# Optimization experiments

Measured on AMD Instinct MI355X. Metric: run time of the kernel, lower is better.

## Reference

```python
import jax, jax.numpy as jnp
import numpy as np

NHEAD = 8
LN_EPS = 1e-5   # torch nn.LayerNorm default
ATT_EPS = 1e-6  # LinearAttention eps


def layernorm(x, g, b):
    mu = jnp.mean(x, axis=-1, keepdims=True)
    var = jnp.mean((x - mu) ** 2, axis=-1, keepdims=True)
    return (x - mu) / jnp.sqrt(var + LN_EPS) * g + b


def setup_inputs() -> dict:
    key = jax.random.key(0)
    ks = jax.random.split(key, 9)
    B, C, H, W = 8, 256, 64, 64
    d = C
    w = lambda k, shp: (jax.random.normal(k, shp, dtype=jnp.float32) * 0.02)
    return {
        "x": jax.random.normal(ks[0], (B, C, H, W), dtype=jnp.float32),
        "source": jax.random.normal(ks[1], (B, C, H, W), dtype=jnp.float32),
        # weights stored [in, out] (already transposed vs torch's [out, in])
        "Wq": w(ks[2], (d, d)),
        "Wk": w(ks[3], (d, d)),
        "Wv": w(ks[4], (d, d)),
        "Wm": w(ks[5], (d, d)),
        "W1": w(ks[6], (2 * d, 2 * d)),
        "W2": w(ks[7], (2 * d, d)),
        "g1": jnp.ones((d,), jnp.float32),
        "b1": jnp.zeros((d,), jnp.float32),
        "g2": jnp.ones((d,), jnp.float32),
        "b2": jnp.zeros((d,), jnp.float32),
    }


def reference(x, source, Wq, Wk, Wv, Wm, W1, W2, g1, b1, g2, b2):
    B, C, H, W = x.shape
    L = H * W
    dim = C // NHEAD
    xs = x.reshape(B, C, L).transpose(0, 2, 1)        # [B, L, C]
    ss = source.reshape(B, C, L).transpose(0, 2, 1)   # [B, L, C]

    q = (xs @ Wq).reshape(B, L, NHEAD, dim)
    k = (ss @ Wk).reshape(B, L, NHEAD, dim)
    v = (ss @ Wv).reshape(B, L, NHEAD, dim)

    # linear attention with elu+1 feature map
    Q = jax.nn.elu(q) + 1.0
    K = jax.nn.elu(k) + 1.0
    vals = v / L
    KV = jnp.einsum('nshd,nshv->nhdv', K, vals)                    # [B, h, d, d]
    Z = 1.0 / (jnp.einsum('nlhd,nhd->nlh', Q, K.sum(axis=1)) + ATT_EPS)
    msg = jnp.einsum('nlhd,nhdv,nlh->nlhv', Q, KV, Z) * L          # [B, L, h, d]

    msg = msg.reshape(B, L, C) @ Wm
    msg = layernorm(msg, g1, b1)
    msg = jax.nn.relu(jnp.concatenate([xs, msg], axis=-1) @ W1) @ W2
    msg = layernorm(msg, g2, b2)

    out = xs + msg
    return out.transpose(0, 2, 1).reshape(B, C, H, W)
```

## Files before the change

### kernel.cpp

```cpp
#include <hip/hip_runtime.h>

typedef unsigned short u16;
typedef __bf16 bf16x8 __attribute__((ext_vector_type(8)));
typedef float f32x4 __attribute__((ext_vector_type(4)));

__device__ __forceinline__ u16 f2bf(float f) {
  unsigned int u = __float_as_uint(f);
  u += 0x7fffu + ((u >> 16) & 1u);
  return (u16)(u >> 16);
}
__device__ __forceinline__ float bf2f(u16 v) {
  return __uint_as_float(((unsigned)v) << 16);
}

#define GLDS16(gp, lp)                                                   \
  __builtin_amdgcn_global_load_lds(                                      \
      (const __attribute__((address_space(1))) unsigned int*)(gp),       \
      (__attribute__((address_space(3))) unsigned int*)(lp), 16, 0, 0)

#define OFF_WQ     0u
#define OFF_WK     131072u
#define OFF_WV     262144u
#define OFF_WM     393216u
#define OFF_W1     524288u
// ... 23 lines not shown
  __syncthreads();
#pragma unroll
  for (int i = 0; i < 4; ++i)
    dst[((size_t)b * 4096 + lt + ty + i * 8) * dstride + ct + tx] = f2bf(s[tx][ty + i * 8]);
}

__global__ __launch_bounds__(256) void wprep_all_kernel(
    const float* __restrict__ Wq, const float* __restrict__ Wk,
    const float* __restrict__ Wv, const float* __restrict__ Wm,
    const float* __restrict__ W1, const float* __restrict__ W2,
    u16* __restrict__ dq, u16* __restrict__ dk, u16* __restrict__ dv,
    u16* __restrict__ dm, u16* __restrict__ d1, u16* __restrict__ d2) {
  __shared__ float s[32][33];
  int bid = blockIdx.x;
  const float* src; u16* dst; int Kd, Nd, t;
  if (bid < 64)       { src = Wq; dst = dq; Kd = 256; Nd = 256; t = bid; }
  else if (bid < 128) { src = Wk; dst = dk; Kd = 256; Nd = 256; t = bid - 64; }
  else if (bid < 192) { src = Wv; dst = dv; Kd = 256; Nd = 256; t = bid - 128; }
  else if (bid < 256) { src = Wm; dst = dm; Kd = 256; Nd = 256; t = bid - 192; }
  else if (bid < 512) { src = W1; dst = d1; Kd = 512; Nd = 512; t = bid - 256; }
  else                { src = W2; dst = d2; Kd = 512; Nd = 256; t = bid - 512; }
  int ntn = Nd >> 5;
  int kt = (t / ntn) * 32, nt = (t % ntn) * 32;
  int tx = threadIdx.x & 31, ty = threadIdx.x >> 5;
#pragma unroll
  for (int i = 0; i < 4; ++i)
    s[ty + i * 8][tx] = src[(size_t)(kt + ty + i * 8) * Nd + nt + tx];
  __syncthreads();
#pragma unroll
  for (int i = 0; i < 4; ++i)
    dst[(size_t)(nt + ty + i * 8) * Kd + kt + tx] = f2bf(s[tx][ty + i * 8]);
}

template <int EPI, int XS>
__global__ __launch_bounds__(256) void gemm_kernel(
    const u16* __restrict__ A, int lda, const u16* __restrict__ Wt, int K,
    u16* __restrict__ outp, int ldo) {
  __shared__ alignas(16) u16 sA[128 * 64];
  __shared__ alignas(16) u16 sB[128 * 64];
  const int tid = threadIdx.x;
  int m0, n0;
  if (XS) {
    int bid = blockIdx.x;
    int xcd = bid & 7, i = bid >> 3;
    m0 = (xcd * 32 + (i >> 2)) * 128;
    n0 = (i & 3) * 128;
  } else {
    m0 = blockIdx.y * 128;
    n0 = blockIdx.x * 128;
  }
  const int w = tid >> 6, lane = tid & 63;
  const int wm = (w >> 1) * 64, wn = (w & 1) * 64;
  const int lr = lane & 15, lk = lane >> 4;
  f32x4 acc[4][4] = {};
  const int srow = tid >> 3, sch = (tid & 7) << 3;
  const u16* ga = A + (size_t)(m0 + srow) * lda + sch;
  const u16* gb = Wt + (size_t)(n0 + srow) * K + sch;

  const int nkt = K >> 6;
  for (int kt = 0; kt < nkt; ++kt) {
    __syncthreads();
#pragma unroll
    for (int i = 0; i < 4; ++i) {
      GLDS16(ga + (size_t)i * 32 * lda + kt * 64, sA + (tid + i * 256) * 8);
      GLDS16(gb + (size_t)i * 32 * K + kt * 64, sB + (tid + i * 256) * 8);
    }
    __syncthreads();
    bf16x8 af[4][2], bfr[4][2];
#pragma unroll
    for (int f = 0; f < 4; ++f) {
#pragma unroll
      for (int ks = 0; ks < 2; ++ks) {
        af[f][ks] = *reinterpret_cast<const bf16x8*>(
            &sA[(wm + f * 16 + lr) * 64 + ks * 32 + lk * 8]);
        bfr[f][ks] = *reinterpret_cast<const bf16x8*>(
            &sB[(wn + f * 16 + lr) * 64 + ks * 32 + lk * 8]);
      }
    }
#pragma unroll
    for (int ks = 0; ks < 2; ++ks)
#pragma unroll
      for (int fm = 0; fm < 4; ++fm)
#pragma unroll
        for (int fn = 0; fn < 4; ++fn)
          acc[fm][fn] = __builtin_amdgcn_mfma_f32_16x16x32_bf16(
              af[fm][ks], bfr[fn][ks], acc[fm][fn], 0, 0, 0);
  }

  const int r0 = (lane >> 4) * 4, c0 = lane & 15;
#pragma unroll
  for (int fm = 0; fm < 4; ++fm) {
#pragma unroll
    for (int fn = 0; fn < 4; ++fn) {
      int gr = m0 + wm + fm * 16 + r0;
      int gc = n0 + wn + fn * 16 + c0;
#pragma unroll
      for (int r = 0; r < 4; ++r) {
        float v = acc[fm][fn][r];
        if (EPI == 3) v = v > 0.f ? v : 0.f;
        if (EPI == 4) v = (gc < 256) ? (v > 0.f ? v + 1.f : __expf(v)) : v * (1.f / 4096.f);
        outp[(size_t)(gr + r) * ldo + gc] = f2bf(v);
      }
    }
  }
}

__global__ __launch_bounds__(256) void kv_partial_kernel(
    const u16* __restrict__ KVproj, float* __restrict__ KVp,
    float* __restrict__ KSp) {
  __shared__ alignas(16) float sK[64][32];
  __shared__ alignas(16) float sV[64][32];
  const int bh = blockIdx.x, sl = blockIdx.y;
  const int b = bh >> 3, h = bh & 7;
  const int t = threadIdx.x;
  const int lrow = t >> 2, lcol = (t & 3) * 8;
  const int d = t >> 3, vg = (t & 7) * 4;
  float a0 = 0, a1 = 0, a2 = 0, a3 = 0, ks = 0;
  for (int lt = 0; lt < 512; lt += 64) {
    __syncthreads();
    size_t roff = ((size_t)b * 4096 + sl * 512 + lt + lrow) * 512 + h * 32 + lcol;
    uint4 kq = *reinterpret_cast<const uint4*>(KVproj + roff);
    uint4 vq = *reinterpret_cast<const uint4*>(KVproj + roff + 256);
    float* dk = &sK[lrow][lcol];
    float* dv = &sV[lrow][lcol];
#pragma unroll
    for (int j = 0; j < 4; ++j) {
      unsigned uk = ((const unsigned*)&kq)[j];
      unsigned uv = ((const unsigned*)&vq)[j];
      dk[2 * j] = __uint_as_float(uk << 16);
      dk[2 * j + 1] = __uint_as_float(uk & 0xffff0000u);
      dv[2 * j] = __uint_as_float(uv << 16);
      dv[2 * j + 1] = __uint_as_float(uv & 0xffff0000u);
// ... 16 lines not shown

__global__ __launch_bounds__(256) void kv_reduce_kernel(
    const float* __restrict__ KVp, const float* __restrict__ KSp,
    float* __restrict__ KV, float* __restrict__ Ksum) {
  int gid = blockIdx.x * 256 + threadIdx.x;
  if (gid < 65536) {
    float s = 0;
#pragma unroll
    for (int i = 0; i < 8; ++i) s += KVp[(size_t)i * 65536 + gid];
    KV[gid] = s;
  } else if (gid - 65536 < 2048) {
    int j = gid - 65536;
    float s = 0;
#pragma unroll
    for (int i = 0; i < 8; ++i) s += KSp[(size_t)i * 2048 + j];
    Ksum[j] = s;
  }
}

__global__ __launch_bounds__(256) void wcomb_kernel(
    const float* __restrict__ KVb, const u16* __restrict__ wmt,
    u16* __restrict__ wc) {
  const int bid = blockIdx.x;
  const int b = bid >> 8, n = bid & 255;
  const int k = threadIdx.x, h = k >> 5, d = k & 31;
  const float* kv = KVb + ((size_t)b * 8 + h) * 1024 + d * 32;
  const u16* wm = wmt + (size_t)n * 256 + h * 32;
  float s = 0.f;
#pragma unroll
  for (int v = 0; v < 32; ++v) s += kv[v] * bf2f(wm[v]);
  wc[((size_t)b * 256 + n) * 256 + k] = f2bf(s);
}

__global__ __launch_bounds__(512) void qproj_fused_kernel(
    const u16* __restrict__ cat, const u16* __restrict__ WqT,
    const float* __restrict__ KSb, u16* __restrict__ Qs) {
  __shared__ alignas(16) u16 sA[128 * 64];
  __shared__ alignas(16) u16 sB[256 * 64];
  const int t = threadIdx.x;
  const int m0 = blockIdx.x * 128;
  const int b = m0 >> 12;
  const int w = t >> 6, lane = t & 63;
  const int wm = (w >> 2) * 64, wn = (w & 3) * 64;
  const int lr = lane & 15, lk = lane >> 4;
  f32x4 acc[4][4] = {};
  float ksv[4];
#pragma unroll
  for (int fn = 0; fn < 4; ++fn) ksv[fn] = KSb[b * 256 + wn + fn * 16 + lr];
  for (int kt = 0; kt < 4; ++kt) {
    __syncthreads();
#pragma unroll
    for (int i = 0; i < 2; ++i) {
      int id = t + i * 512, row = id >> 3, chn = (id & 7) << 3;
      GLDS16(cat + (size_t)(m0 + row) * 512 + kt * 64 + chn, sA + id * 8);
    }
#pragma unroll
    for (int i = 0; i < 4; ++i) {
      int id = t + i * 512, row = id >> 3, chn = (id & 7) << 3;
      GLDS16(WqT + (size_t)row * 256 + kt * 64 + chn, sB + id * 8);
    }
    __syncthreads();
    bf16x8 af[4][2], bfr[4][2];
#pragma unroll
    for (int f = 0; f < 4; ++f) {
#pragma unroll
      for (int ks = 0; ks < 2; ++ks) {
        af[f][ks] = *reinterpret_cast<const bf16x8*>(
            &sA[(wm + f * 16 + lr) * 64 + ks * 32 + lk * 8]);
        bfr[f][ks] = *reinterpret_cast<const bf16x8*>(
            &sB[(wn + f * 16 + lr) * 64 + ks * 32 + lk * 8]);
      }
    }
#pragma unroll
    for (int ks = 0; ks < 2; ++ks)
#pragma unroll
      for (int fm = 0; fm < 4; ++fm)
#pragma unroll
        for (int fn = 0; fn < 4; ++fn)
          acc[fm][fn] = __builtin_amdgcn_mfma_f32_16x16x32_bf16(
              af[fm][ks], bfr[fn][ks], acc[fm][fn], 0, 0, 0);
  }
#pragma unroll
  for (int fm = 0; fm < 4; ++fm)
#pragma unroll
    for (int r = 0; r < 4; ++r) {
      float q[4];
#pragma unroll
      for (int fn = 0; fn < 4; ++fn) {
        float v = acc[fm][fn][r];
        q[fn] = v > 0.f ? v + 1.f : __expf(v);
      }
      float zd0 = q[0] * ksv[0] + q[1] * ksv[1];
      float zd1 = q[2] * ksv[2] + q[3] * ksv[3];
#pragma unroll
      for (int off = 1; off < 16; off <<= 1) {
        zd0 += __shfl_xor(zd0, off);
        zd1 += __shfl_xor(zd1, off);
      }
      float z0 = 4096.f / (zd0 + 1e-6f);
      float z1 = 4096.f / (zd1 + 1e-6f);
      size_t row = (size_t)(m0 + wm + fm * 16 + lk * 4 + r) * 256;
      Qs[row + wn + lr] = f2bf(q[0] * z0);
      Qs[row + wn + 16 + lr] = f2bf(q[1] * z0);
      Qs[row + wn + 32 + lr] = f2bf(q[2] * z1);
      Qs[row + wn + 48 + lr] = f2bf(q[3] * z1);
    }
}

__global__ __launch_bounds__(512) void msgwm_ln1_kernel(
    const u16* __restrict__ Qs, const u16* __restrict__ wc,
    const float* __restrict__ g1, const float* __restrict__ b1,
    u16* __restrict__ cat) {
  __shared__ alignas(16) char smem[49152 + 4096 + 2048];
  u16* sA = (u16*)smem;
  u16* sB = (u16*)(smem + 16384);
  float* scr = (float*)(smem + 49152);
  float* sG = (float*)(smem + 53248);
  u16* T = (u16*)smem;
  const int t = threadIdx.x;
  const int m0 = blockIdx.x * 128;
  const int b = m0 >> 12;
  const u16* Bw = wc + (size_t)b * 65536;
  if (t < 256) { sG[t] = g1[t]; sG[256 + t] = b1[t]; }
  const int w = t >> 6, lane = t & 63;
  const int wm = (w >> 2) * 64, wn = (w & 3) * 64;
  const int lr = lane & 15, lk = lane >> 4;
  f32x4 acc[4][4] = {};
  for (int kt = 0; kt < 4; ++kt) {
    __syncthreads();
#pragma unroll
    for (int i = 0; i < 2; ++i) {
      int id = t + i * 512, row = id >> 3, chn = (id & 7) << 3;
      GLDS16(Qs + (size_t)(m0 + row) * 256 + kt * 64 + chn, sA + id * 8);
    }
#pragma unroll
    for (int i = 0; i < 4; ++i) {
      int id = t + i * 512, row = id >> 3, chn = (id & 7) << 3;
      GLDS16(Bw + (size_t)row * 256 + kt * 64 + chn, sB + id * 8);
    }
    __syncthreads();
    bf16x8 af[4][2], bfr[4][2];
#pragma unroll
    for (int f = 0; f < 4; ++f) {
#pragma unroll
      for (int ks = 0; ks < 2; ++ks) {
        af[f][ks] = *reinterpret_cast<const bf16x8*>(
            &sA[(wm + f * 16 + lr) * 64 + ks * 32 + lk * 8]);
        bfr[f][ks] = *reinterpret_cast<const bf16x8*>(
            &sB[(wn + f * 16 + lr) * 64 + ks * 32 + lk * 8]);
      }
    }
#pragma unroll
    for (int ks = 0; ks < 2; ++ks)
#pragma unroll
      for (int fm = 0; fm < 4; ++fm)
#pragma unroll
        for (int fn = 0; fn < 4; ++fn)
          acc[fm][fn] = __builtin_amdgcn_mfma_f32_16x16x32_bf16(
              af[fm][ks], bfr[fn][ks], acc[fm][fn], 0, 0, 0);
  }
#pragma unroll
  for (int fm = 0; fm < 4; ++fm)
#pragma unroll
    for (int r = 0; r < 4; ++r) {
      float s = 0.f, sq = 0.f;
#pragma unroll
      for (int fn = 0; fn < 4; ++fn) {
        float a = acc[fm][fn][r];
        s += a; sq += a * a;
      }
#pragma unroll
      for (int off = 1; off < 16; off <<= 1) {
        s += __shfl_xor(s, off);
        sq += __shfl_xor(sq, off);
      }
      if (lr == 0) {
        int row = wm + fm * 16 + lk * 4 + r;
        scr[row * 8 + (w & 3) * 2] = s;
        scr[row * 8 + (w & 3) * 2 + 1] = sq;
      }
    }
  __syncthreads();
  float gvs[4], bvs[4];
#pragma unroll
  for (int fn = 0; fn < 4; ++fn) {
    gvs[fn] = sG[wn + fn * 16 + lr];
    bvs[fn] = sG[256 + wn + fn * 16 + lr];
  }
#pragma unroll
  for (int fm = 0; fm < 4; ++fm)
#pragma unroll
    for (int r = 0; r < 4; ++r) {
      int row = wm + fm * 16 + lk * 4 + r;
      float s = 0.f, sq = 0.f;
#pragma unroll
      for (int j = 0; j < 4; ++j) {
        s += scr[row * 8 + j * 2];
        sq += scr[row * 8 + j * 2 + 1];
      }
      float mu = s * (1.f / 256.f);
      float var = sq * (1.f / 256.f) - mu * mu;
      float rstd = rsqrtf(var + 1e-5f);
#pragma unroll
      for (int fn = 0; fn < 4; ++fn)
        acc[fm][fn][r] = (acc[fm][fn][r] - mu) * rstd * gvs[fn] + bvs[fn];
    }
  for (int hh = 0; hh < 2; ++hh) {
    __syncthreads();
    if ((w >> 2) == hh) {
#pragma unroll
      for (int fm = 0; fm < 4; ++fm)
#pragma unroll
        for (int fn = 0; fn < 4; ++fn)
#pragma unroll
          for (int r = 0; r < 4; ++r)
            T[(fm * 16 + lk * 4 + r) * 264 + wn + fn * 16 + lr] =
                f2bf(acc[fm][fn][r]);
    }
    __syncthreads();
#pragma unroll
    for (int i = 0; i < 4; ++i) {
      int idx = t + i * 512;
      int row = idx >> 5, c16 = idx & 31;
      uint4 val = *reinterpret_cast<const uint4*>(&T[row * 264 + c16 * 8]);
      *reinterpret_cast<uint4*>(
          cat + (size_t)(m0 + hh * 64 + row) * 512 + 256 + c16 * 8) = val;
    }
  }
}

__global__ __launch_bounds__(512) void mlp2_tail_kernel(
    const u16* __restrict__ hidden, const u16* __restrict__ W2T,
    const float* __restrict__ g2, const float* __restrict__ b2,
    const u16* __restrict__ catp, float* __restrict__ out) {
  __shared__ alignas(16) char smem[16384 + 32768 + 4096 + 2048];
  u16* sA = (u16*)smem;
  u16* sB = (u16*)(smem + 16384);
  float* scr = (float*)(smem + 49152);
  float* sG = (float*)(smem + 53248);
  float* T = (float*)smem;
  const int t = threadIdx.x;
  const int m0 = blockIdx.x * 128;
  const int b = m0 >> 12, l0 = m0 & 4095;
  if (t < 256) { sG[t] = g2[t]; sG[256 + t] = b2[t]; }
  const int w = t >> 6, lane = t & 63;
  const int wm = (w >> 2) * 64, wn = (w & 3) * 64;
  const int lr = lane & 15, lk = lane >> 4;
  f32x4 acc[4][4] = {};
  for (int kt = 0; kt < 8; ++kt) {
    __syncthreads();
#pragma unroll
    for (int i = 0; i < 2; ++i) {
      int id = t + i * 512, row = id >> 3, chn = (id & 7) << 3;
      GLDS16(hidden + (size_t)(m0 + row) * 512 + kt * 64 + chn, sA + id * 8);
    }
#pragma unroll
    for (int i = 0; i < 4; ++i) {
      int id = t + i * 512, row = id >> 3, chn = (id & 7) << 3;
      GLDS16(W2T + (size_t)row * 512 + kt * 64 + chn, sB + id * 8);
    }
    __syncthreads();
    bf16x8 af[4][2], bfr[4][2];
#pragma unroll
    for (int f = 0; f < 4; ++f) {
#pragma unroll
      for (int ks = 0; ks < 2; ++ks) {
        af[f][ks] = *reinterpret_cast<const bf16x8*>(
            &sA[(wm + f * 16 + lr) * 64 + ks * 32 + lk * 8]);
        bfr[f][ks] = *reinterpret_cast<const bf16x8*>(
            &sB[(wn + f * 16 + lr) * 64 + ks * 32 + lk * 8]);
      }
    }
#pragma unroll
    for (int ks = 0; ks < 2; ++ks)
#pragma unroll
      for (int fm = 0; fm < 4; ++fm)
#pragma unroll
        for (int fn = 0; fn < 4; ++fn)
          acc[fm][fn] = __builtin_amdgcn_mfma_f32_16x16x32_bf16(
              af[fm][ks], bfr[fn][ks], acc[fm][fn], 0, 0, 0);
  }
#pragma unroll
  for (int fm = 0; fm < 4; ++fm)
#pragma unroll
    for (int r = 0; r < 4; ++r) {
      float s = 0.f, sq = 0.f;
#pragma unroll
      for (int fn = 0; fn < 4; ++fn) {
        float a = acc[fm][fn][r];
        s += a; sq += a * a;
      }
#pragma unroll
      for (int off = 1; off < 16; off <<= 1) {
        s += __shfl_xor(s, off);
        sq += __shfl_xor(sq, off);
      }
      if (lr == 0) {
        int row = wm + fm * 16 + lk * 4 + r;
        scr[row * 8 + (w & 3) * 2] = s;
        scr[row * 8 + (w & 3) * 2 + 1] = sq;
      }
    }
  __syncthreads();
  float gvs[4], bvs[4];
#pragma unroll
  for (int fn = 0; fn < 4; ++fn) {
    gvs[fn] = sG[wn + fn * 16 + lr];
    bvs[fn] = sG[256 + wn + fn * 16 + lr];
  }
#pragma unroll
  for (int fm = 0; fm < 4; ++fm)
#pragma unroll
    for (int r = 0; r < 4; ++r) {
      int row = wm + fm * 16 + lk * 4 + r;
      float s = 0.f, sq = 0.f;
#pragma unroll
      for (int j = 0; j < 4; ++j) {
        s += scr[row * 8 + j * 2];
        sq += scr[row * 8 + j * 2 + 1];
      }
      float mu = s * (1.f / 256.f);
      float var = sq * (1.f / 256.f) - mu * mu;
      float rstd = rsqrtf(var + 1e-5f);
#pragma unroll
      for (int fn = 0; fn < 4; ++fn) {
        float xs = bf2f(catp[(size_t)(m0 + row) * 512 + wn + fn * 16 + lr]);
        acc[fm][fn][r] = (acc[fm][fn][r] - mu) * rstd * gvs[fn] + bvs[fn] + xs;
      }
    }
  __syncthreads();
  for (int cc = 0; cc < 4; ++cc) {
    if ((w & 3) == cc) {
#pragma unroll
      for (int fm = 0; fm < 4; ++fm)
#pragma unroll
        for (int fn = 0; fn < 4; ++fn)
#pragma unroll
          for (int r = 0; r < 4; ++r)
            T[(fn * 16 + lr) * 129 + wm + fm * 16 + lk * 4 + r] = acc[fm][fn][r];
    }
    __syncthreads();
#pragma unroll
    for (int i = 0; i < 4; ++i) {
      int idx = t + i * 512;
      int cT = idx >> 5, lq = (idx & 31) * 4;
      int cg = cc * 64 + cT;
      size_t o = ((size_t)b * 256 + cg) * 4096 + l0 + lq;
      float4 ov;
      ov.x = T[cT * 129 + lq];
      ov.y = T[cT * 129 + lq + 1];
      ov.z = T[cT * 129 + lq + 2];
      ov.w = T[cT * 129 + lq + 3];
      *reinterpret_cast<float4*>(out + o) = ov;
    }
    __syncthreads();
  }
}

extern "C" void kernel_launch(void* const* d_in, const int* in_sizes, int n_in,
                              void* d_out, int out_size, void* d_ws, size_t ws_size,
                              hipStream_t stream) {
  (void)in_sizes; (void)n_in; (void)out_size; (void)ws_size;
  const float* x = (const float*)d_in[0];
  const float* srcp = (const float*)d_in[1];
  const float* Wq = (const float*)d_in[2];
  const float* Wk = (const float*)d_in[3];
  const float* Wv = (const float*)d_in[4];
  const float* Wm = (const float*)d_in[5];
  const float* W1 = (const float*)d_in[6];
  const float* W2 = (const float*)d_in[7];
  const float* g1 = (const float*)d_in[8];
  const float* b1 = (const float*)d_in[9];
  const float* g2 = (const float*)d_in[10];
  const float* b2 = (const float*)d_in[11];
  float* out = (float*)d_out;
  char* ws = (char*)d_ws;

  u16* wqt = (u16*)(ws + OFF_WQ);
  u16* wkvt = (u16*)(ws + OFF_WK);
  u16* wkt = (u16*)(ws + OFF_WK);
  u16* wvt = (u16*)(ws + OFF_WV);
  u16* wmt = (u16*)(ws + OFF_WM);
  u16* w1t = (u16*)(ws + OFF_W1);
  u16* w2t = (u16*)(ws + OFF_W2);
  u16* cat = (u16*)(ws + OFF_CAT);
  u16* ssb = (u16*)(ws + OFF_SSB);
  u16* kvproj = (u16*)(ws + OFF_KVPROJ);
  float* KVb = (float*)(ws + OFF_KV);
  float* KSb = (float*)(ws + OFF_KS);
  float* KVp = (float*)(ws + OFF_KVP);
  float* KSp = (float*)(ws + OFF_KSP);
  u16* hidden = kvproj;
  u16* Qs = ssb;
  u16* wcombT = (u16*)(ws + OFF_KVP);

  dim3 blk(256);
  wprep_all_kernel<<<dim3(640), blk, 0, stream>>>(Wq, Wk, Wv, Wm, W1, W2,
                                                  wqt, wkt, wvt, wmt, w1t, w2t);
  transpose_in_kernel<<<dim3(128, 8, 16), blk, 0, stream>>>(x, srcp, cat, ssb);
  gemm_kernel<4, 1><<<dim3(1024), blk, 0, stream>>>(ssb, 256, wkvt, 256, kvproj, 512);
  kv_partial_kernel<<<dim3(64, 8), blk, 0, stream>>>(kvproj, KVp, KSp);
  kv_reduce_kernel<<<dim3(264), blk, 0, stream>>>(KVp, KSp, KVb, KSb);
  qproj_fused_kernel<<<dim3(256), dim3(512), 0, stream>>>(cat, wqt, KSb, Qs);
  wcomb_kernel<<<dim3(2048), blk, 0, stream>>>(KVb, wmt, wcombT);
  msgwm_ln1_kernel<<<dim3(256), dim3(512), 0, stream>>>(Qs, wcombT, g1, b1, cat);
  gemm_kernel<3, 1><<<dim3(1024), blk, 0, stream>>>(cat, 512, w1t, 512, hidden, 512);
  mlp2_tail_kernel<<<dim3(256), dim3(512), 0, stream>>>(hidden, w2t, g2, b2, cat, out);
}
```

Baseline: 175.8 us.

## Fuse Q-projection with message GEMM and fuse both MLP GEMMs per row tile

Merges the Q projection and normalisation kernel with the message/Wm/LayerNorm1 kernel, keeping the normalised Q tile in LDS instead of writing and rereading it from global memory. Likewise fuses the W1 GEMM with ReLU and the W2 GEMM with LayerNorm2 and the transposed output store, holding the hidden activations in LDS chunk by chunk. This removes two intermediate global round trips and two launches, but uses smaller 64- and 32-row tiles, which means more repeated weight loads per block, more syncs, and scalar rather than float4 output stores.

```diff
diff --git a/kernel.cpp b/kernel.cpp
--- a/kernel.cpp
+++ b/kernel.cpp
@@ -79,23 +79,17 @@
     dst[(size_t)(nt + ty + i * 8) * Kd + kt + tx] = f2bf(s[tx][ty + i * 8]);
 }
 
-template <int EPI, int XS>
+template <int EPI>
 __global__ __launch_bounds__(256) void gemm_kernel(
     const u16* __restrict__ A, int lda, const u16* __restrict__ Wt, int K,
     u16* __restrict__ outp, int ldo) {
   __shared__ alignas(16) u16 sA[128 * 64];
   __shared__ alignas(16) u16 sB[128 * 64];
   const int tid = threadIdx.x;
-  int m0, n0;
-  if (XS) {
-    int bid = blockIdx.x;
-    int xcd = bid & 7, i = bid >> 3;
-    m0 = (xcd * 32 + (i >> 2)) * 128;
-    n0 = (i & 3) * 128;
-  } else {
-    m0 = blockIdx.y * 128;
-    n0 = blockIdx.x * 128;
-  }
+  int bid = blockIdx.x;
+  int xcd = bid & 7, i0 = bid >> 3;
+  const int m0 = (xcd * 32 + (i0 >> 2)) * 128;
+  const int n0 = (i0 & 3) * 128;
   const int w = tid >> 6, lane = tid & 63;
   const int wm = (w >> 1) * 64, wn = (w & 1) * 64;
   const int lr = lane & 15, lk = lane >> 4;
@@ -144,7 +138,6 @@
 #pragma unroll
       for (int r = 0; r < 4; ++r) {
         float v = acc[fm][fn][r];
-        if (EPI == 3) v = v > 0.f ? v : 0.f;
         if (EPI == 4) v = (gc < 256) ? (v > 0.f ? v + 1.f : __expf(v)) : v * (1.f / 4096.f);
         outp[(size_t)(gr + r) * ldo + gc] = f2bf(v);
       }
@@ -227,17 +220,24 @@
   wc[((size_t)b * 256 + n) * 256 + k] = f2bf(s);
 }
 
-__global__ __launch_bounds__(512) void qproj_fused_kernel(
+__global__ __launch_bounds__(256) void qmsg_kernel(
     const u16* __restrict__ cat, const u16* __restrict__ WqT,
-    const float* __restrict__ KSb, u16* __restrict__ Qs) {
-  __shared__ alignas(16) u16 sA[128 * 64];
-  __shared__ alignas(16) u16 sB[256 * 64];
+    const float* __restrict__ KSb, const u16* __restrict__ wc,
+    const float* __restrict__ g1, const float* __restrict__ b1,
+    u16* __restrict__ catout) {
+  __shared__ alignas(16) char smem[57344];
+  u16* sA = (u16*)smem;
+  u16* sB = (u16*)(smem + 8192);
+  u16* Qlds = (u16*)smem;
+  float* scr = (float*)(smem + 33280);
+  u16* sWc = (u16*)(smem + 40960);
+  u16* T = (u16*)smem;
   const int t = threadIdx.x;
-  const int m0 = blockIdx.x * 128;
+  const int m0 = blockIdx.x * 64;
   const int b = m0 >> 12;
   const int w = t >> 6, lane = t & 63;
-  const int wm = (w >> 2) * 64, wn = (w & 3) * 64;
   const int lr = lane & 15, lk = lane >> 4;
+  const int wn = w * 64;
   f32x4 acc[4][4] = {};
   float ksv[4];
 #pragma unroll
@@ -246,26 +246,23 @@
     __syncthreads();
 #pragma unroll
     for (int i = 0; i < 2; ++i) {
-      int id = t + i * 512, row = id >> 3, chn = (id & 7) << 3;
-      GLDS16(cat + (size_t)(m0 + row) * 512 + kt * 64 + chn, sA + id * 8);
-    }
-#pragma unroll
-    for (int i = 0; i < 4; ++i) {
-      int id = t + i * 512, row = id >> 3, chn = (id & 7) << 3;
-      GLDS16(WqT + (size_t)row * 256 + kt * 64 + chn, sB + id * 8);
+      int id = t + i * 256, row = id >> 3, ch = (id & 7) * 8;
+      GLDS16(cat + (size_t)(m0 + row) * 512 + kt * 64 + ch, sA + id * 8);
+    }
+#pragma unroll
+    for (int i = 0; i < 8; ++i) {
+      int id = t + i * 256, row = id >> 3, ch = (id & 7) * 8;
+      GLDS16(WqT + (size_t)row * 256 + kt * 64 + ch, sB + id * 8);
     }
     __syncthreads();
     bf16x8 af[4][2], bfr[4][2];
 #pragma unroll
-    for (int f = 0; f < 4; ++f) {
+    for (int f = 0; f < 4; ++f)
 #pragma unroll
       for (int ks = 0; ks < 2; ++ks) {
-        af[f][ks] = *reinterpret_cast<const bf16x8*>(
-            &sA[(wm + f * 16 + lr) * 64 + ks * 32 + lk * 8]);
-        bfr[f][ks] = *reinterpret_cast<const bf16x8*>(
-            &sB[(wn + f * 16 + lr) * 64 + ks * 32 + lk * 8]);
-      }
-    }
+        af[f][ks] = *(const bf16x8*)&sA[(f * 16 + lr) * 64 + ks * 32 + lk * 8];
+        bfr[f][ks] = *(const bf16x8*)&sB[(wn + f * 16 + lr) * 64 + ks * 32 + lk * 8];
+      }
 #pragma unroll
     for (int ks = 0; ks < 2; ++ks)
 #pragma unroll
@@ -294,65 +291,42 @@
       }
       float z0 = 4096.f / (zd0 + 1e-6f);
       float z1 = 4096.f / (zd1 + 1e-6f);
-      size_t row = (size_t)(m0 + wm + fm * 16 + lk * 4 + r) * 256;
-      Qs[row + wn + lr] = f2bf(q[0] * z0);
-      Qs[row + wn + 16 + lr] = f2bf(q[1] * z0);
-      Qs[row + wn + 32 + lr] = f2bf(q[2] * z1);
-      Qs[row + wn + 48 + lr] = f2bf(q[3] * z1);
-    }
-}
-
-__global__ __launch_bounds__(512) void msgwm_ln1_kernel(
-    const u16* __restrict__ Qs, const u16* __restrict__ wc,
-    const float* __restrict__ g1, const float* __restrict__ b1,
-    u16* __restrict__ cat) {
-  __shared__ alignas(16) char smem[49152 + 4096 + 2048];
-  u16* sA = (u16*)smem;
-  u16* sB = (u16*)(smem + 16384);
-  float* scr = (float*)(smem + 49152);
-  float* sG = (float*)(smem + 53248);
-  u16* T = (u16*)smem;
-  const int t = threadIdx.x;
-  const int m0 = blockIdx.x * 128;
-  const int b = m0 >> 12;
+      acc[fm][0][r] = q[0] * z0; acc[fm][1][r] = q[1] * z0;
+      acc[fm][2][r] = q[2] * z1; acc[fm][3][r] = q[3] * z1;
+    }
+  __syncthreads();
+#pragma unroll
+  for (int fm = 0; fm < 4; ++fm)
+#pragma unroll
+    for (int fn = 0; fn < 4; ++fn)
+#pragma unroll
+      for (int r = 0; r < 4; ++r)
+        Qlds[(fm * 16 + lk * 4 + r) * 260 + wn + fn * 16 + lr] = f2bf(acc[fm][fn][r]);
+  f32x4 acc2[4][4] = {};
   const u16* Bw = wc + (size_t)b * 65536;
-  if (t < 256) { sG[t] = g1[t]; sG[256 + t] = b1[t]; }
-  const int w = t >> 6, lane = t & 63;
-  const int wm = (w >> 2) * 64, wn = (w & 3) * 64;
-  const int lr = lane & 15, lk = lane >> 4;
-  f32x4 acc[4][4] = {};
-  for (int kt = 0; kt < 4; ++kt) {
-    __syncthreads();
-#pragma unroll
-    for (int i = 0; i < 2; ++i) {
-      int id = t + i * 512, row = id >> 3, chn = (id & 7) << 3;
-      GLDS16(Qs + (size_t)(m0 + row) * 256 + kt * 64 + chn, sA + id * 8);
-    }
+  for (int kc = 0; kc < 8; ++kc) {
+    __syncthreads();
 #pragma unroll
     for (int i = 0; i < 4; ++i) {
-      int id = t + i * 512, row = id >> 3, chn = (id & 7) << 3;
-      GLDS16(Bw + (size_t)row * 256 + kt * 64 + chn, sB + id * 8);
-    }
-    __syncthreads();
-    bf16x8 af[4][2], bfr[4][2];
-#pragma unroll
-    for (int f = 0; f < 4; ++f) {
-#pragma unroll
-      for (int ks = 0; ks < 2; ++ks) {
-        af[f][ks] = *reinterpret_cast<const bf16x8*>(
-            &sA[(wm + f * 16 + lr) * 64 + ks * 32 + lk * 8]);
-        bfr[f][ks] = *reinterpret_cast<const bf16x8*>(
-            &sB[(wn + f * 16 + lr) * 64 + ks * 32 + lk * 8]);
-      }
-    }
-#pragma unroll
-    for (int ks = 0; ks < 2; ++ks)
-#pragma unroll
-      for (int fm = 0; fm < 4; ++fm)
-#pragma unroll
-        for (int fn = 0; fn < 4; ++fn)
-          acc[fm][fn] = __builtin_amdgcn_mfma_f32_16x16x32_bf16(
-              af[fm][ks], bfr[fn][ks], acc[fm][fn], 0, 0, 0);
+      int id = t + i * 256, row = id >> 2, ch = (id & 3) * 8;
+      GLDS16(Bw + (size_t)row * 256 + kc * 32 + (ch ^ ((row & 3) << 3)), sWc + id * 8);
+    }
+    __syncthreads();
+    bf16x8 a2[4], b2f[4];
+#pragma unroll
+    for (int f = 0; f < 4; ++f)
+      a2[f] = *(const bf16x8*)&Qlds[(f * 16 + lr) * 260 + kc * 32 + lk * 8];
+#pragma unroll
+    for (int fn = 0; fn < 4; ++fn) {
+      int br = wn + fn * 16 + lr;
+      b2f[fn] = *(const bf16x8*)&sWc[br * 32 + ((lk * 8) ^ ((br & 3) << 3))];
+    }
+#pragma unroll
+    for (int fm = 0; fm < 4; ++fm)
+#pragma unroll
+      for (int fn = 0; fn < 4; ++fn)
+        acc2[fm][fn] = __builtin_amdgcn_mfma_f32_16x16x32_bf16(
+            a2[fm], b2f[fn], acc2[fm][fn], 0, 0, 0);
   }
 #pragma unroll
   for (int fm = 0; fm < 4; ++fm)
@@ -361,7 +335,7 @@
       float s = 0.f, sq = 0.f;
 #pragma unroll
       for (int fn = 0; fn < 4; ++fn) {
-        float a = acc[fm][fn][r];
+        float a = acc2[fm][fn][r];
         s += a; sq += a * a;
       }
 #pragma unroll
@@ -370,23 +344,23 @@
         sq += __shfl_xor(sq, off);
       }
       if (lr == 0) {
-        int row = wm + fm * 16 + lk * 4 + r;
-        scr[row * 8 + (w & 3) * 2] = s;
-        scr[row * 8 + (w & 3) * 2 + 1] = sq;
+        int row = fm * 16 + lk * 4 + r;
+        scr[row * 8 + w * 2] = s;
+        scr[row * 8 + w * 2 + 1] = sq;
       }
     }
   __syncthreads();
   float gvs[4], bvs[4];
 #pragma unroll
   for (int fn = 0; fn < 4; ++fn) {
-    gvs[fn] = sG[wn + fn * 16 + lr];
-    bvs[fn] = sG[256 + wn + fn * 16 + lr];
+    gvs[fn] = g1[wn + fn * 16 + lr];
+    bvs[fn] = b1[wn + fn * 16 + lr];
   }
 #pragma unroll
   for (int fm = 0; fm < 4; ++fm)
 #pragma unroll
     for (int r = 0; r < 4; ++r) {
-      int row = wm + fm * 16 + lk * 4 + r;
+      int row = fm * 16 + lk * 4 + r;
       float s = 0.f, sq = 0.f;
 #pragma unroll
       for (int j = 0; j < 4; ++j) {
@@ -397,92 +371,117 @@
       float var = sq * (1.f / 256.f) - mu * mu;
       float rstd = rsqrtf(var + 1e-5f);
 #pragma unroll
-      for (int fn = 0; fn < 4; ++fn)
-        acc[fm][fn][r] = (acc[fm][fn][r] - mu) * rstd * gvs[fn] + bvs[fn];
-    }
-  for (int hh = 0; hh < 2; ++hh) {
-    __syncthreads();
-    if ((w >> 2) == hh) {
-#pragma unroll
-      for (int fm = 0; fm < 4; ++fm)
-#pragma unroll
-        for (int fn = 0; fn < 4; ++fn)
-#pragma unroll
-          for (int r = 0; r < 4; ++r)
-            T[(fm * 16 + lk * 4 + r) * 264 + wn + fn * 16 + lr] =
-                f2bf(acc[fm][fn][r]);
-    }
-    __syncthreads();
-#pragma unroll
-    for (int i = 0; i < 4; ++i) {
-      int idx = t + i * 512;
-      int row = idx >> 5, c16 = idx & 31;
-      uint4 val = *reinterpret_cast<const uint4*>(&T[row * 264 + c16 * 8]);
-      *reinterpret_cast<uint4*>(
-          cat + (size_t)(m0 + hh * 64 + row) * 512 + 256 + c16 * 8) = val;
-    }
-  }
-}
-
-__global__ __launch_bounds__(512) void mlp2_tail_kernel(
-    const u16* __restrict__ hidden, const u16* __restrict__ W2T,
-    const float* __restrict__ g2, const float* __restrict__ b2,
-    const u16* __restrict__ catp, float* __restrict__ out) {
-  __shared__ alignas(16) char smem[16384 + 32768 + 4096 + 2048];
-  u16* sA = (u16*)smem;
-  u16* sB = (u16*)(smem + 16384);
-  float* scr = (float*)(smem + 49152);
-  float* sG = (float*)(smem + 53248);
+      for (int fn = 0; fn < 4; ++fn) {
+        float y = (acc2[fm][fn][r] - mu) * rstd * gvs[fn] + bvs[fn];
+        T[(fm * 16 + lk * 4 + r) * 260 + wn + fn * 16 + lr] = f2bf(y);
+      }
+    }
+  __syncthreads();
+#pragma unroll
+  for (int i = 0; i < 8; ++i) {
+    int idx = t + i * 256;
+    int row = idx >> 5, c16 = idx & 31;
+    uint4 val = *reinterpret_cast<const uint4*>(&T[row * 260 + c16 * 8]);
+    *reinterpret_cast<uint4*>(catout + (size_t)(m0 + row) * 512 + 256 + c16 * 8) = val;
+  }
+}
+
+__global__ __launch_bounds__(256) void mlp_fused_kernel(
+    const u16* __restrict__ cat, const u16* __restrict__ W1T,
+    const u16* __restrict__ W2T, const float* __restrict__ g2,
+    const float* __restrict__ b2, float* __restrict__ out) {
+  __shared__ alignas(16) char smem[58880];
+  u16* sX = (u16*)smem;
+  u16* sW = (u16*)(smem + 32768);
+  u16* sH = (u16*)(smem + 49152);
+  float* scr = (float*)(smem + 57856);
   float* T = (float*)smem;
   const int t = threadIdx.x;
-  const int m0 = blockIdx.x * 128;
+  const int m0 = blockIdx.x * 32;
   const int b = m0 >> 12, l0 = m0 & 4095;
-  if (t < 256) { sG[t] = g2[t]; sG[256 + t] = b2[t]; }
   const int w = t >> 6, lane = t & 63;
-  const int wm = (w >> 2) * 64, wn = (w & 3) * 64;
   const int lr = lane & 15, lk = lane >> 4;
-  f32x4 acc[4][4] = {};
-  for (int kt = 0; kt < 8; ++kt) {
-    __syncthreads();
-#pragma unroll
-    for (int i = 0; i < 2; ++i) {
-      int id = t + i * 512, row = id >> 3, chn = (id & 7) << 3;
-      GLDS16(hidden + (size_t)(m0 + row) * 512 + kt * 64 + chn, sA + id * 8);
-    }
-#pragma unroll
-    for (int i = 0; i < 4; ++i) {
-      int id = t + i * 512, row = id >> 3, chn = (id & 7) << 3;
-      GLDS16(W2T + (size_t)row * 512 + kt * 64 + chn, sB + id * 8);
-    }
-    __syncthreads();
-    bf16x8 af[4][2], bfr[4][2];
-#pragma unroll
-    for (int f = 0; f < 4; ++f) {
-#pragma unroll
-      for (int ks = 0; ks < 2; ++ks) {
-        af[f][ks] = *reinterpret_cast<const bf16x8*>(
-            &sA[(wm + f * 16 + lr) * 64 + ks * 32 + lk * 8]);
-        bfr[f][ks] = *reinterpret_cast<const bf16x8*>(
-            &sB[(wn + f * 16 + lr) * 64 + ks * 32 + lk * 8]);
-      }
-    }
-#pragma unroll
-    for (int ks = 0; ks < 2; ++ks)
-#pragma unroll
-      for (int fm = 0; fm < 4; ++fm)
+  const int wn1 = w * 32, wn2 = w * 64;
+#pragma unroll
+  for (int i = 0; i < 8; ++i) {
+    int id = t + i * 256;
+    int row = id >> 6, ch = (id & 63) * 8;
+    GLDS16(cat + (size_t)(m0 + row) * 512 + (ch ^ ((row & 7) << 3)), sX + id * 8);
+  }
+  f32x4 acc2[2][4] = {};
+  for (int nc = 0; nc < 4; ++nc) {
+    f32x4 acc1[2][2] = {};
+    for (int kc = 0; kc < 8; ++kc) {
+      __syncthreads();
+#pragma unroll
+      for (int i = 0; i < 4; ++i) {
+        int id = t + i * 256, row = id >> 3, ch = (id & 7) * 8;
+        GLDS16(W1T + (size_t)(nc * 128 + row) * 512 + kc * 64 + ch, sW + id * 8);
+      }
+      __syncthreads();
+      bf16x8 a1[2][2], b1f[2][2];
+#pragma unroll
+      for (int f = 0; f < 2; ++f)
+#pragma unroll
+        for (int ks = 0; ks < 2; ++ks) {
+          int ar = f * 16 + lr;
+          a1[f][ks] = *(const bf16x8*)&sX[ar * 512 +
+              ((kc * 64 + ks * 32 + lk * 8) ^ ((ar & 7) << 3))];
+          b1f[f][ks] = *(const bf16x8*)&sW[(wn1 + f * 16 + lr) * 64 + ks * 32 + lk * 8];
+        }
+#pragma unroll
+      for (int ks = 0; ks < 2; ++ks)
+#pragma unroll
+        for (int fm = 0; fm < 2; ++fm)
+#pragma unroll
+          for (int fn = 0; fn < 2; ++fn)
+            acc1[fm][fn] = __builtin_amdgcn_mfma_f32_16x16x32_bf16(
+                a1[fm][ks], b1f[fn][ks], acc1[fm][fn], 0, 0, 0);
+    }
+#pragma unroll
+    for (int fm = 0; fm < 2; ++fm)
+#pragma unroll
+      for (int fn = 0; fn < 2; ++fn)
+#pragma unroll
+        for (int r = 0; r < 4; ++r) {
+          float v = acc1[fm][fn][r];
+          sH[(fm * 16 + lk * 4 + r) * 136 + wn1 + fn * 16 + lr] =
+              f2bf(v > 0.f ? v : 0.f);
+        }
+    for (int kc2 = 0; kc2 < 4; ++kc2) {
+      __syncthreads();
+#pragma unroll
+      for (int i = 0; i < 4; ++i) {
+        int id = t + i * 256, row = id >> 2, ch = (id & 3) * 8;
+        GLDS16(W2T + (size_t)row * 512 + nc * 128 + kc2 * 32 +
+                   (ch ^ ((row & 3) << 3)), sW + id * 8);
+      }
+      __syncthreads();
+      bf16x8 a2[2], b2f[4];
+#pragma unroll
+      for (int f = 0; f < 2; ++f)
+        a2[f] = *(const bf16x8*)&sH[(f * 16 + lr) * 136 + kc2 * 32 + lk * 8];
+#pragma unroll
+      for (int fn = 0; fn < 4; ++fn) {
+        int br = wn2 + fn * 16 + lr;
+        b2f[fn] = *(const bf16x8*)&sW[br * 32 + ((lk * 8) ^ ((br & 3) << 3))];
+      }
+#pragma unroll
+      for (int fm = 0; fm < 2; ++fm)
 #pragma unroll
         for (int fn = 0; fn < 4; ++fn)
-          acc[fm][fn] = __builtin_amdgcn_mfma_f32_16x16x32_bf16(
-              af[fm][ks], bfr[fn][ks], acc[fm][fn], 0, 0, 0);
-  }
-#pragma unroll
-  for (int fm = 0; fm < 4; ++fm)
+          acc2[fm][fn] = __builtin_amdgcn_mfma_f32_16x16x32_bf16(
+              a2[fm], b2f[fn], acc2[fm][fn], 0, 0, 0);
+    }
+  }
+#pragma unroll
+  for (int fm = 0; fm < 2; ++fm)
 #pragma unroll
     for (int r = 0; r < 4; ++r) {
       float s = 0.f, sq = 0.f;
 #pragma unroll
       for (int fn = 0; fn < 4; ++fn) {
-        float a = acc[fm][fn][r];
+        float a = acc2[fm][fn][r];
         s += a; sq += a * a;
       }
 #pragma unroll
@@ -491,23 +490,23 @@
         sq += __shfl_xor(sq, off);
       }
       if (lr == 0) {
-        int row = wm + fm * 16 + lk * 4 + r;
-        scr[row * 8 + (w & 3) * 2] = s;
-        scr[row * 8 + (w & 3) * 2 + 1] = sq;
+        int row = fm * 16 + lk * 4 + r;
+        scr[row * 8 + w * 2] = s;
+        scr[row * 8 + w * 2 + 1] = sq;
       }
     }
   __syncthreads();
   float gvs[4], bvs[4];
 #pragma unroll
   for (int fn = 0; fn < 4; ++fn) {
-    gvs[fn] = sG[wn + fn * 16 + lr];
-    bvs[fn] = sG[256 + wn + fn * 16 + lr];
-  }
-#pragma unroll
-  for (int fm = 0; fm < 4; ++fm)
+    gvs[fn] = g2[wn2 + fn * 16 + lr];
+    bvs[fn] = b2[wn2 + fn * 16 + lr];
+  }
+#pragma unroll
+  for (int fm = 0; fm < 2; ++fm)
 #pragma unroll
     for (int r = 0; r < 4; ++r) {
-      int row = wm + fm * 16 + lk * 4 + r;
+      int row = fm * 16 + lk * 4 + r;
       float s = 0.f, sq = 0.f;
 #pragma unroll
       for (int j = 0; j < 4; ++j) {
@@ -519,34 +518,27 @@
       float rstd = rsqrtf(var + 1e-5f);
 #pragma unroll
       for (int fn = 0; fn < 4; ++fn) {
-        float xs = bf2f(catp[(size_t)(m0 + row) * 512 + wn + fn * 16 + lr]);
-        acc[fm][fn][r] = (acc[fm][fn][r] - mu) * rstd * gvs[fn] + bvs[fn] + xs;
+        float xs = bf2f(cat[(size_t)(m0 + row) * 512 + wn2 + fn * 16 + lr]);
+        acc2[fm][fn][r] = (acc2[fm][fn][r] - mu) * rstd * gvs[fn] + bvs[fn] + xs;
       }
     }
   __syncthreads();
   for (int cc = 0; cc < 4; ++cc) {
-    if ((w & 3) == cc) {
-#pragma unroll
-      for (int fm = 0; fm < 4; ++fm)
+    if (w == cc) {
+#pragma unroll
+      for (int fm = 0; fm < 2; ++fm)
 #pragma unroll
         for (int fn = 0; fn < 4; ++fn)
 #pragma unroll
           for (int r = 0; r < 4; ++r)
-            T[(fn * 16 + lr) * 129 + wm + fm * 16 + lk * 4 + r] = acc[fm][fn][r];
-    }
-    __syncthreads();
-#pragma unroll
-    for (int i = 0; i < 4; ++i) {
-      int idx = t + i * 512;
-      int cT = idx >> 5, lq = (idx & 31) * 4;
-      int cg = cc * 64 + cT;
-      size_t o = ((size_t)b * 256 + cg) * 4096 + l0 + lq;
-      float4 ov;
-      ov.x = T[cT * 129 + lq];
-      ov.y = T[cT * 129 + lq + 1];
-      ov.z = T[cT * 129 + lq + 2];
-      ov.w = T[cT * 129 + lq + 3];
-      *reinterpret_cast<float4*>(out + o) = ov;
+            T[(fn * 16 + lr) * 33 + fm * 16 + lk * 4 + r] = acc2[fm][fn][r];
+    }
+    __syncthreads();
+#pragma unroll
+    for (int i = 0; i < 8; ++i) {
+      int idx = t + i * 256;
+      int cT = idx >> 5, lq = idx & 31;
+      out[((size_t)b * 256 + cc * 64 + cT) * 4096 + l0 + lq] = T[cT * 33 + lq];
     }
     __syncthreads();
   }
@@ -585,20 +577,16 @@
   float* KSb = (float*)(ws + OFF_KS);
   float* KVp = (float*)(ws + OFF_KVP);
   float* KSp = (float*)(ws + OFF_KSP);
-  u16* hidden = kvproj;
-  u16* Qs = ssb;
   u16* wcombT = (u16*)(ws + OFF_KVP);
 
   dim3 blk(256);
   wprep_all_kernel<<<dim3(640), blk, 0, stream>>>(Wq, Wk, Wv, Wm, W1, W2,
                                                   wqt, wkt, wvt, wmt, w1t, w2t);
   transpose_in_kernel<<<dim3(128, 8, 16), blk, 0, stream>>>(x, srcp, cat, ssb);
-  gemm_kernel<4, 1><<<dim3(1024), blk, 0, stream>>>(ssb, 256, wkvt, 256, kvproj, 512);
+  gemm_kernel<4><<<dim3(1024), blk, 0, stream>>>(ssb, 256, wkvt, 256, kvproj, 512);
   kv_partial_kernel<<<dim3(64, 8), blk, 0, stream>>>(kvproj, KVp, KSp);
   kv_reduce_kernel<<<dim3(264), blk, 0, stream>>>(KVp, KSp, KVb, KSb);
-  qproj_fused_kernel<<<dim3(256), dim3(512), 0, stream>>>(cat, wqt, KSb, Qs);
   wcomb_kernel<<<dim3(2048), blk, 0, stream>>>(KVb, wmt, wcombT);
-  msgwm_ln1_kernel<<<dim3(256), dim3(512), 0, stream>>>(Qs, wcombT, g1, b1, cat);
-  gemm_kernel<3, 1><<<dim3(1024), blk, 0, stream>>>(cat, 512, w1t, 512, hidden, 512);
-  mlp2_tail_kernel<<<dim3(256), dim3(512), 0, stream>>>(hidden, w2t, g2, b2, cat, out);
-}
+  qmsg_kernel<<<dim3(512), blk, 0, stream>>>(cat, wqt, KSb, wcombT, g1, b1, cat);
+  mlp_fused_kernel<<<dim3(1024), blk, 0, stream>>>(cat, w1t, w2t, g2, b2, out);
+}
```

Result: slower. 186.6 us (+6.2%).

## Fuse Q projection with message/Wm/LN1 GEMM and widen generic GEMM tiles

Applied to the files above, without the earlier changes.

Merges the Q-projection kernel and the message×Wcomb+LayerNorm kernel into one kernel. The normalized Q tile now stays in LDS and feeds the second GEMM directly instead of round-tripping through global memory. The new kernel uses 64-row tiles, 256 threads and a swizzled LDS layout for the Wcomb chunks. The generic GEMM is switched to 128x256 tiles with 512 threads, halving the block count and reusing each A tile across more output columns. The fused kernel trades occupancy and larger LDS use for removing one launch and the Qs write/read traffic.

```diff
diff --git a/kernel.cpp b/kernel.cpp
--- a/kernel.cpp
+++ b/kernel.cpp
@@ -79,38 +79,33 @@
     dst[(size_t)(nt + ty + i * 8) * Kd + kt + tx] = f2bf(s[tx][ty + i * 8]);
 }
 
-template <int EPI, int XS>
-__global__ __launch_bounds__(256) void gemm_kernel(
+template <int EPI>
+__global__ __launch_bounds__(512) void gemm256_kernel(
     const u16* __restrict__ A, int lda, const u16* __restrict__ Wt, int K,
     u16* __restrict__ outp, int ldo) {
   __shared__ alignas(16) u16 sA[128 * 64];
-  __shared__ alignas(16) u16 sB[128 * 64];
-  const int tid = threadIdx.x;
-  int m0, n0;
-  if (XS) {
-    int bid = blockIdx.x;
-    int xcd = bid & 7, i = bid >> 3;
-    m0 = (xcd * 32 + (i >> 2)) * 128;
-    n0 = (i & 3) * 128;
-  } else {
-    m0 = blockIdx.y * 128;
-    n0 = blockIdx.x * 128;
-  }
-  const int w = tid >> 6, lane = tid & 63;
-  const int wm = (w >> 1) * 64, wn = (w & 1) * 64;
+  __shared__ alignas(16) u16 sB[256 * 64];
+  const int t = threadIdx.x;
+  int bid = blockIdx.x;
+  int xcd = bid & 7, i0 = bid >> 3;
+  const int m0 = (xcd * 32 + (i0 >> 1)) * 128;
+  const int n0 = (i0 & 1) * 256;
+  const int w = t >> 6, lane = t & 63;
+  const int wm = (w >> 2) * 64, wn = (w & 3) * 64;
   const int lr = lane & 15, lk = lane >> 4;
   f32x4 acc[4][4] = {};
-  const int srow = tid >> 3, sch = (tid & 7) << 3;
-  const u16* ga = A + (size_t)(m0 + srow) * lda + sch;
-  const u16* gb = Wt + (size_t)(n0 + srow) * K + sch;
-
   const int nkt = K >> 6;
   for (int kt = 0; kt < nkt; ++kt) {
     __syncthreads();
 #pragma unroll
+    for (int i = 0; i < 2; ++i) {
+      int id = t + i * 512, row = id >> 3, ch = (id & 7) << 3;
+      GLDS16(A + (size_t)(m0 + row) * lda + kt * 64 + ch, sA + id * 8);
+    }
+#pragma unroll
     for (int i = 0; i < 4; ++i) {
-      GLDS16(ga + (size_t)i * 32 * lda + kt * 64, sA + (tid + i * 256) * 8);
-      GLDS16(gb + (size_t)i * 32 * K + kt * 64, sB + (tid + i * 256) * 8);
+      int id = t + i * 512, row = id >> 3, ch = (id & 7) << 3;
+      GLDS16(Wt + (size_t)(n0 + row) * K + kt * 64 + ch, sB + id * 8);
     }
     __syncthreads();
     bf16x8 af[4][2], bfr[4][2];
@@ -133,7 +128,6 @@
           acc[fm][fn] = __builtin_amdgcn_mfma_f32_16x16x32_bf16(
               af[fm][ks], bfr[fn][ks], acc[fm][fn], 0, 0, 0);
   }
-
   const int r0 = (lane >> 4) * 4, c0 = lane & 15;
 #pragma unroll
   for (int fm = 0; fm < 4; ++fm) {
@@ -227,17 +221,24 @@
   wc[((size_t)b * 256 + n) * 256 + k] = f2bf(s);
 }
 
-__global__ __launch_bounds__(512) void qproj_fused_kernel(
+__global__ __launch_bounds__(256) void qmsg_kernel(
     const u16* __restrict__ cat, const u16* __restrict__ WqT,
-    const float* __restrict__ KSb, u16* __restrict__ Qs) {
-  __shared__ alignas(16) u16 sA[128 * 64];
-  __shared__ alignas(16) u16 sB[256 * 64];
+    const float* __restrict__ KSb, const u16* __restrict__ wc,
+    const float* __restrict__ g1, const float* __restrict__ b1,
+    u16* __restrict__ catout) {
+  __shared__ alignas(16) char smem[57344];
+  u16* sA = (u16*)smem;
+  u16* sB = (u16*)(smem + 8192);
+  u16* Qlds = (u16*)smem;
+  float* scr = (float*)(smem + 33280);
+  u16* sWc = (u16*)(smem + 40960);
+  u16* T = (u16*)smem;
   const int t = threadIdx.x;
-  const int m0 = blockIdx.x * 128;
+  const int m0 = blockIdx.x * 64;
   const int b = m0 >> 12;
   const int w = t >> 6, lane = t & 63;
-  const int wm = (w >> 2) * 64, wn = (w & 3) * 64;
   const int lr = lane & 15, lk = lane >> 4;
+  const int wn = w * 64;
   f32x4 acc[4][4] = {};
   float ksv[4];
 #pragma unroll
@@ -246,26 +247,23 @@
     __syncthreads();
 #pragma unroll
     for (int i = 0; i < 2; ++i) {
-      int id = t + i * 512, row = id >> 3, chn = (id & 7) << 3;
-      GLDS16(cat + (size_t)(m0 + row) * 512 + kt * 64 + chn, sA + id * 8);
-    }
-#pragma unroll
-    for (int i = 0; i < 4; ++i) {
-      int id = t + i * 512, row = id >> 3, chn = (id & 7) << 3;
-      GLDS16(WqT + (size_t)row * 256 + kt * 64 + chn, sB + id * 8);
+      int id = t + i * 256, row = id >> 3, ch = (id & 7) * 8;
+      GLDS16(cat + (size_t)(m0 + row) * 512 + kt * 64 + ch, sA + id * 8);
+    }
+#pragma unroll
+    for (int i = 0; i < 8; ++i) {
+      int id = t + i * 256, row = id >> 3, ch = (id & 7) * 8;
+      GLDS16(WqT + (size_t)row * 256 + kt * 64 + ch, sB + id * 8);
     }
     __syncthreads();
     bf16x8 af[4][2], bfr[4][2];
 #pragma unroll
-    for (int f = 0; f < 4; ++f) {
+    for (int f = 0; f < 4; ++f)
 #pragma unroll
       for (int ks = 0; ks < 2; ++ks) {
-        af[f][ks] = *reinterpret_cast<const bf16x8*>(
-            &sA[(wm + f * 16 + lr) * 64 + ks * 32 + lk * 8]);
-        bfr[f][ks] = *reinterpret_cast<const bf16x8*>(
-            &sB[(wn + f * 16 + lr) * 64 + ks * 32 + lk * 8]);
-      }
-    }
+        af[f][ks] = *(const bf16x8*)&sA[(f * 16 + lr) * 64 + ks * 32 + lk * 8];
+        bfr[f][ks] = *(const bf16x8*)&sB[(wn + f * 16 + lr) * 64 + ks * 32 + lk * 8];
+      }
 #pragma unroll
     for (int ks = 0; ks < 2; ++ks)
 #pragma unroll
@@ -294,65 +292,42 @@
       }
       float z0 = 4096.f / (zd0 + 1e-6f);
       float z1 = 4096.f / (zd1 + 1e-6f);
-      size_t row = (size_t)(m0 + wm + fm * 16 + lk * 4 + r) * 256;
-      Qs[row + wn + lr] = f2bf(q[0] * z0);
-      Qs[row + wn + 16 + lr] = f2bf(q[1] * z0);
-      Qs[row + wn + 32 + lr] = f2bf(q[2] * z1);
-      Qs[row + wn + 48 + lr] = f2bf(q[3] * z1);
-    }
-}
-
-__global__ __launch_bounds__(512) void msgwm_ln1_kernel(
-    const u16* __restrict__ Qs, const u16* __restrict__ wc,
-    const float* __restrict__ g1, const float* __restrict__ b1,
-    u16* __restrict__ cat) {
-  __shared__ alignas(16) char smem[49152 + 4096 + 2048];
-  u16* sA = (u16*)smem;
-  u16* sB = (u16*)(smem + 16384);
-  float* scr = (float*)(smem + 49152);
-  float* sG = (float*)(smem + 53248);
-  u16* T = (u16*)smem;
-  const int t = threadIdx.x;
-  const int m0 = blockIdx.x * 128;
-  const int b = m0 >> 12;
+      acc[fm][0][r] = q[0] * z0; acc[fm][1][r] = q[1] * z0;
+      acc[fm][2][r] = q[2] * z1; acc[fm][3][r] = q[3] * z1;
+    }
+  __syncthreads();
+#pragma unroll
+  for (int fm = 0; fm < 4; ++fm)
+#pragma unroll
+    for (int fn = 0; fn < 4; ++fn)
+#pragma unroll
+      for (int r = 0; r < 4; ++r)
+        Qlds[(fm * 16 + lk * 4 + r) * 260 + wn + fn * 16 + lr] = f2bf(acc[fm][fn][r]);
+  f32x4 acc2[4][4] = {};
   const u16* Bw = wc + (size_t)b * 65536;
-  if (t < 256) { sG[t] = g1[t]; sG[256 + t] = b1[t]; }
-  const int w = t >> 6, lane = t & 63;
-  const int wm = (w >> 2) * 64, wn = (w & 3) * 64;
-  const int lr = lane & 15, lk = lane >> 4;
-  f32x4 acc[4][4] = {};
-  for (int kt = 0; kt < 4; ++kt) {
-    __syncthreads();
-#pragma unroll
-    for (int i = 0; i < 2; ++i) {
-      int id = t + i * 512, row = id >> 3, chn = (id & 7) << 3;
-      GLDS16(Qs + (size_t)(m0 + row) * 256 + kt * 64 + chn, sA + id * 8);
-    }
+  for (int kc = 0; kc < 8; ++kc) {
+    __syncthreads();
 #pragma unroll
     for (int i = 0; i < 4; ++i) {
-      int id = t + i * 512, row = id >> 3, chn = (id & 7) << 3;
-      GLDS16(Bw + (size_t)row * 256 + kt * 64 + chn, sB + id * 8);
-    }
-    __syncthreads();
-    bf16x8 af[4][2], bfr[4][2];
-#pragma unroll
-    for (int f = 0; f < 4; ++f) {
-#pragma unroll
-      for (int ks = 0; ks < 2; ++ks) {
-        af[f][ks] = *reinterpret_cast<const bf16x8*>(
-            &sA[(wm + f * 16 + lr) * 64 + ks * 32 + lk * 8]);
-        bfr[f][ks] = *reinterpret_cast<const bf16x8*>(
-            &sB[(wn + f * 16 + lr) * 64 + ks * 32 + lk * 8]);
-      }
-    }
-#pragma unroll
-    for (int ks = 0; ks < 2; ++ks)
-#pragma unroll
-      for (int fm = 0; fm < 4; ++fm)
-#pragma unroll
-        for (int fn = 0; fn < 4; ++fn)
-          acc[fm][fn] = __builtin_amdgcn_mfma_f32_16x16x32_bf16(
-              af[fm][ks], bfr[fn][ks], acc[fm][fn], 0, 0, 0);
+      int id = t + i * 256, row = id >> 2, ch = (id & 3) * 8;
+      GLDS16(Bw + (size_t)row * 256 + kc * 32 + (ch ^ ((row & 3) << 3)), sWc + id * 8);
+    }
+    __syncthreads();
+    bf16x8 a2[4], b2f[4];
+#pragma unroll
+    for (int f = 0; f < 4; ++f)
+      a2[f] = *(const bf16x8*)&Qlds[(f * 16 + lr) * 260 + kc * 32 + lk * 8];
+#pragma unroll
+    for (int fn = 0; fn < 4; ++fn) {
+      int br = wn + fn * 16 + lr;
+      b2f[fn] = *(const bf16x8*)&sWc[br * 32 + ((lk * 8) ^ ((br & 3) << 3))];
+    }
+#pragma unroll
+    for (int fm = 0; fm < 4; ++fm)
+#pragma unroll
+      for (int fn = 0; fn < 4; ++fn)
+        acc2[fm][fn] = __builtin_amdgcn_mfma_f32_16x16x32_bf16(
+            a2[fm], b2f[fn], acc2[fm][fn], 0, 0, 0);
   }
 #pragma unroll
   for (int fm = 0; fm < 4; ++fm)
@@ -361,7 +336,7 @@
       float s = 0.f, sq = 0.f;
 #pragma unroll
       for (int fn = 0; fn < 4; ++fn) {
-        float a = acc[fm][fn][r];
+        float a = acc2[fm][fn][r];
         s += a; sq += a * a;
       }
 #pragma unroll
@@ -370,23 +345,23 @@
         sq += __shfl_xor(sq, off);
       }
       if (lr == 0) {
-        int row = wm + fm * 16 + lk * 4 + r;
-        scr[row * 8 + (w & 3) * 2] = s;
-        scr[row * 8 + (w & 3) * 2 + 1] = sq;
+        int row = fm * 16 + lk * 4 + r;
+        scr[row * 8 + w * 2] = s;
+        scr[row * 8 + w * 2 + 1] = sq;
       }
     }
   __syncthreads();
   float gvs[4], bvs[4];
 #pragma unroll
   for (int fn = 0; fn < 4; ++fn) {
-    gvs[fn] = sG[wn + fn * 16 + lr];
-    bvs[fn] = sG[256 + wn + fn * 16 + lr];
+    gvs[fn] = g1[wn + fn * 16 + lr];
+    bvs[fn] = b1[wn + fn * 16 + lr];
   }
 #pragma unroll
   for (int fm = 0; fm < 4; ++fm)
 #pragma unroll
     for (int r = 0; r < 4; ++r) {
-      int row = wm + fm * 16 + lk * 4 + r;
+      int row = fm * 16 + lk * 4 + r;
       float s = 0.f, sq = 0.f;
 #pragma unroll
       for (int j = 0; j < 4; ++j) {
@@ -397,30 +372,18 @@
       float var = sq * (1.f / 256.f) - mu * mu;
       float rstd = rsqrtf(var + 1e-5f);
 #pragma unroll
-      for (int fn = 0; fn < 4; ++fn)
-        acc[fm][fn][r] = (acc[fm][fn][r] - mu) * rstd * gvs[fn] + bvs[fn];
-    }
-  for (int hh = 0; hh < 2; ++hh) {
-    __syncthreads();
-    if ((w >> 2) == hh) {
-#pragma unroll
-      for (int fm = 0; fm < 4; ++fm)
-#pragma unroll
-        for (int fn = 0; fn < 4; ++fn)
-#pragma unroll
-          for (int r = 0; r < 4; ++r)
-            T[(fm * 16 + lk * 4 + r) * 264 + wn + fn * 16 + lr] =
-                f2bf(acc[fm][fn][r]);
-    }
-    __syncthreads();
-#pragma unroll
-    for (int i = 0; i < 4; ++i) {
-      int idx = t + i * 512;
-      int row = idx >> 5, c16 = idx & 31;
-      uint4 val = *reinterpret_cast<const uint4*>(&T[row * 264 + c16 * 8]);
-      *reinterpret_cast<uint4*>(
-          cat + (size_t)(m0 + hh * 64 + row) * 512 + 256 + c16 * 8) = val;
-    }
+      for (int fn = 0; fn < 4; ++fn) {
+        float y = (acc2[fm][fn][r] - mu) * rstd * gvs[fn] + bvs[fn];
+        T[(fm * 16 + lk * 4 + r) * 260 + wn + fn * 16 + lr] = f2bf(y);
+      }
+    }
+  __syncthreads();
+#pragma unroll
+  for (int i = 0; i < 8; ++i) {
+    int idx = t + i * 256;
+    int row = idx >> 5, c16 = idx & 31;
+    uint4 val = *reinterpret_cast<const uint4*>(&T[row * 260 + c16 * 8]);
+    *reinterpret_cast<uint4*>(catout + (size_t)(m0 + row) * 512 + 256 + c16 * 8) = val;
   }
 }
 
@@ -586,19 +549,17 @@
   float* KVp = (float*)(ws + OFF_KVP);
   float* KSp = (float*)(ws + OFF_KSP);
   u16* hidden = kvproj;
-  u16* Qs = ssb;
   u16* wcombT = (u16*)(ws + OFF_KVP);
 
   dim3 blk(256);
   wprep_all_kernel<<<dim3(640), blk, 0, stream>>>(Wq, Wk, Wv, Wm, W1, W2,
                                                   wqt, wkt, wvt, wmt, w1t, w2t);
   transpose_in_kernel<<<dim3(128, 8, 16), blk, 0, stream>>>(x, srcp, cat, ssb);
-  gemm_kernel<4, 1><<<dim3(1024), blk, 0, stream>>>(ssb, 256, wkvt, 256, kvproj, 512);
+  gemm256_kernel<4><<<dim3(512), dim3(512), 0, stream>>>(ssb, 256, wkvt, 256, kvproj, 512);
   kv_partial_kernel<<<dim3(64, 8), blk, 0, stream>>>(kvproj, KVp, KSp);
   kv_reduce_kernel<<<dim3(264), blk, 0, stream>>>(KVp, KSp, KVb, KSb);
-  qproj_fused_kernel<<<dim3(256), dim3(512), 0, stream>>>(cat, wqt, KSb, Qs);
   wcomb_kernel<<<dim3(2048), blk, 0, stream>>>(KVb, wmt, wcombT);
-  msgwm_ln1_kernel<<<dim3(256), dim3(512), 0, stream>>>(Qs, wcombT, g1, b1, cat);
-  gemm_kernel<3, 1><<<dim3(1024), blk, 0, stream>>>(cat, 512, w1t, 512, hidden, 512);
+  qmsg_kernel<<<dim3(512), blk, 0, stream>>>(cat, wqt, KSb, wcombT, g1, b1, cat);
+  gemm256_kernel<3><<<dim3(512), dim3(512), 0, stream>>>(cat, 512, w1t, 512, hidden, 512);
   mlp2_tail_kernel<<<dim3(256), dim3(512), 0, stream>>>(hidden, w2t, g2, b2, cat, out);
 }
```

After: 161.1 us. 8.3% less time.
